# Kernel optimization log

Hardware: AMD Instinct MI355X
Metric: run time of the kernel (lower is better)

## Reference

```python
import jax, jax.numpy as jnp
import numpy as np

KSIZE = (3, 3, 3)
STRIDE = (2, 2, 2)
PAD = (1, 1, 1)
DIL = (1, 1, 1)


def _box_sum(x):
    # Sum over a (kT,kH,kW) window with stride/padding/dilation, applied over
    # the last 3 dims of a [N, C, T, H, W] tensor (equivalent to conv3d with a
    # ones kernel applied channel-wise).
    return jax.lax.reduce_window(
        x,
        jnp.array(0.0, x.dtype),
        jax.lax.add,
        window_dimensions=(1, 1) + KSIZE,
        window_strides=(1, 1) + STRIDE,
        padding=((0, 0), (0, 0)) + tuple((p, p) for p in PAD),
        window_dilation=(1, 1) + DIL,
    )


def setup_inputs() -> dict:
    key = jax.random.key(0)
    k1, k2 = jax.random.split(key)
    vw = jax.random.normal(k1, (4, 256, 16, 56, 56), dtype=jnp.float32)
    w = jax.random.normal(k2, (4, 16, 256), dtype=jnp.float32)
    return {"vw": vw, "w": w}


def reference(vw, w):
    # vw: [N, C, T, H, W] visual words; w: [N, K, C] language words
    C = vw.shape[1]
    # per-word dot products (the 1x1x1 conv3d in the original): [N, K, T, H, W]
    dotp = jnp.einsum('nkc,ncthw->nkthw', w, vw)
    # aggregate over words (op='max'), keepdim -> [N, 1, T, H, W]
    agg = jnp.max(dotp, axis=1, keepdims=True)
    emap = jnp.exp(agg / np.float32(np.sqrt(C)))
    # box-filter sum of exp map -> denominator [N, 1, T', H', W']
    denom = _box_sum(emap)
    # box-filter sum of exp-weighted features -> numerator [N, C, T', H', W']
    num = _box_sum(vw * emap)
    return num / denom
```

## Files before the change

### kernel.cpp

```cpp
#include <hip/hip_runtime.h>
#include <hip/hip_bf16.h>

#define N_  4
#define C_  256
#define K_  16
#define T_  16
#define H_  56
#define W_  56
#define HW_ (H_ * W_)
#define THW_ (T_ * HW_)
#define TP_ 8
#define HP_ 28
#define WP_ 28
#define PP_ (HP_ * WP_)
#define CCHUNK 8

__global__ __launch_bounds__(256) void emap_kernel(const float* __restrict__ vw,
                                                   const float* __restrict__ w,
                                                   float* __restrict__ emap) {
    __shared__ float wl[K_ * C_];
    const int tid = threadIdx.x;
    const int bpn = THW_ / (256 * 2);
    const int n = blockIdx.x / bpn;
    const int lb = blockIdx.x % bpn;

    const float* wn = w + n * (K_ * C_);
#pragma unroll
    for (int i = 0; i < K_; ++i) wl[i * C_ + tid] = wn[i * C_ + tid];
    __syncthreads();

    const int s = (lb * 256 + tid) * 2;
    const float* vbase = vw + (long)n * C_ * THW_ + s;

    float acc0[K_], acc1[K_];
#pragma unroll
    for (int k = 0; k < K_; ++k) { acc0[k] = 0.f; acc1[k] = 0.f; }

    for (int c4 = 0; c4 < C_; c4 += 4) {
        float2 v0 = *(const float2*)(vbase + (long)(c4 + 0) * THW_);
        float2 v1 = *(const float2*)(vbase + (long)(c4 + 1) * THW_);
        float2 v2 = *(const float2*)(vbase + (long)(c4 + 2) * THW_);
        float2 v3 = *(const float2*)(vbase + (long)(c4 + 3) * THW_);
#pragma unroll
        for (int k = 0; k < K_; ++k) {
            float4 wk = *(const float4*)&wl[k * C_ + c4];
            acc0[k] += wk.x * v0.x + wk.y * v1.x + wk.z * v2.x + wk.w * v3.x;
            acc1[k] += wk.x * v0.y + wk.y * v1.y + wk.z * v2.y + wk.w * v3.y;
        }
    }

    float m0 = acc0[0], m1 = acc1[0];
#pragma unroll
    for (int k = 1; k < K_; ++k) { m0 = fmaxf(m0, acc0[k]); m1 = fmaxf(m1, acc1[k]); }

    float2 e;
    e.x = expf(m0 * 0.0625f);
    e.y = expf(m1 * 0.0625f);
    *(float2*)(emap + (long)n * THW_ + s) = e;
}

__global__ __launch_bounds__(256) void box_kernel(const float* __restrict__ vw,
                                                  const float* __restrict__ emap,
                                                  float* __restrict__ out) {
    __shared__ float se[3 * HW_];
    __shared__ float sden[PP_];

    const int tid = threadIdx.x;
    const int cb = blockIdx.x * CCHUNK;
    const int tp = blockIdx.y;
    const int n  = blockIdx.z;
    const int t0 = 2 * tp - 1;

    for (int sl = 0; sl < 3; ++sl) {
        const int tt = t0 + sl;
        if (tt >= 0) {
            const float* src = emap + (long)n * THW_ + (long)tt * HW_;
            for (int i = tid; i < HW_; i += 256) se[sl * HW_ + i] = src[i];
        } else {
            for (int i = tid; i < HW_; i += 256) se[sl * HW_ + i] = 0.f;
        }
    }
    __syncthreads();

    for (int p = tid; p < PP_; p += 256) {
        const int hp = p / WP_, wp = p % WP_;
        const int h0 = 2 * hp - 1, w0 = 2 * wp - 1;
        float ssum = 0.f;
#pragma unroll
        for (int dt = 0; dt < 3; ++dt) {
#pragma unroll
            for (int dh = 0; dh < 3; ++dh) {
                const int h = h0 + dh;
                if (h < 0) continue;
#pragma unroll
                for (int dw = 0; dw < 3; ++dw) {
                    const int w = w0 + dw;
                    if (w < 0) continue;
                    ssum += se[dt * HW_ + h * W_ + w];
                }
            }
        }
        sden[p] = 1.0f / ssum;
    }
    __syncthreads();

    for (int idx = tid; idx < CCHUNK * PP_; idx += 256) {
        const int c = cb + idx / PP_;
        const int p = idx % PP_;
        const int hp = p / WP_, wp = p % WP_;
        const int h0 = 2 * hp - 1, w0 = 2 * wp - 1;
        const float* vbase = vw + ((long)n * C_ + c) * THW_;
        float num = 0.f;
#pragma unroll
        for (int dt = 0; dt < 3; ++dt) {
            const int tt = t0 + dt;
            if (tt < 0) continue;
            const float* vt = vbase + (long)tt * HW_;
            const float* et = se + dt * HW_;
#pragma unroll
            for (int dh = 0; dh < 3; ++dh) {
                const int h = h0 + dh;
                if (h < 0) continue;
#pragma unroll
                for (int dw = 0; dw < 3; ++dw) {
                    const int w = w0 + dw;
                    if (w < 0) continue;
                    const int o = h * W_ + w;
                    num += vt[o] * et[o];
                }
            }
        }
        out[(((long)n * C_ + c) * TP_ + tp) * PP_ + p] = num * sden[p];
    }
}

extern "C" void kernel_launch(void* const* d_in, const int* in_sizes, int n_in,
                              void* d_out, int out_size, void* d_ws, size_t ws_size,
                              hipStream_t stream) {
    const float* vw = (const float*)d_in[0];
    const float* w  = (const float*)d_in[1];
    float* out  = (float*)d_out;
    float* emap = (float*)d_ws;

    emap_kernel<<<392, 256, 0, stream>>>(vw, w, emap);

    box_kernel<<<dim3(C_ / CCHUNK, TP_, N_), 256, 0, stream>>>(vw, emap, out);
}
```

Baseline: 416.8 us.

## Split emap channel reduction across waves and restructure box kernel per output position

The emap kernel now splits the 256-channel dot product across four waves, each covering 64 channels. Partial sums are reduced through shared memory and launched over four times as many blocks, which raises parallelism and occupancy; weights are read directly from global memory instead of being staged in LDS. The box kernel drops the shared-memory staging of three emap slices. Each thread now owns one output position, keeps its 27 emap values and offsets in registers, and loops over 16 channels, so the denominator is computed once per thread and reused. The trade-off is higher register pressure and uncached global gathers of vw with stride-2 access.

```diff
diff --git a/kernel.cpp b/kernel.cpp
--- a/kernel.cpp
+++ b/kernel.cpp
@@ -13,124 +13,115 @@
 #define HP_ 28
 #define WP_ 28
 #define PP_ (HP_ * WP_)
-#define CCHUNK 8
+#define CB_ 16
 
 __global__ __launch_bounds__(256) void emap_kernel(const float* __restrict__ vw,
                                                    const float* __restrict__ w,
                                                    float* __restrict__ emap) {
-    __shared__ float wl[K_ * C_];
-    const int tid = threadIdx.x;
-    const int bpn = THW_ / (256 * 2);
-    const int n = blockIdx.x / bpn;
-    const int lb = blockIdx.x % bpn;
+    __shared__ float part[K_][4][128];
+    const int tid  = threadIdx.x;
+    const int wave = tid >> 6;
+    const int lane = tid & 63;
+    const int bpn  = THW_ / 128;
+    const int n    = blockIdx.x / bpn;
+    const int s0   = (blockIdx.x % bpn) * 128;
+    const int s    = s0 + lane * 2;
 
-    const float* wn = w + n * (K_ * C_);
+    const float* vbase = vw + (long)(n * C_ + wave * 64) * THW_ + s;
+    const float* wn    = w + n * (K_ * C_) + wave * 64;
+
+    float a0[K_], a1[K_];
 #pragma unroll
-    for (int i = 0; i < K_; ++i) wl[i * C_ + tid] = wn[i * C_ + tid];
-    __syncthreads();
+    for (int k = 0; k < K_; ++k) { a0[k] = 0.f; a1[k] = 0.f; }
 
-    const int s = (lb * 256 + tid) * 2;
-    const float* vbase = vw + (long)n * C_ * THW_ + s;
-
-    float acc0[K_], acc1[K_];
-#pragma unroll
-    for (int k = 0; k < K_; ++k) { acc0[k] = 0.f; acc1[k] = 0.f; }
-
-    for (int c4 = 0; c4 < C_; c4 += 4) {
-        float2 v0 = *(const float2*)(vbase + (long)(c4 + 0) * THW_);
-        float2 v1 = *(const float2*)(vbase + (long)(c4 + 1) * THW_);
-        float2 v2 = *(const float2*)(vbase + (long)(c4 + 2) * THW_);
-        float2 v3 = *(const float2*)(vbase + (long)(c4 + 3) * THW_);
+    for (int c = 0; c < 64; c += 4) {
+        float2 v0 = *(const float2*)(vbase + (long)(c + 0) * THW_);
+        float2 v1 = *(const float2*)(vbase + (long)(c + 1) * THW_);
+        float2 v2 = *(const float2*)(vbase + (long)(c + 2) * THW_);
+        float2 v3 = *(const float2*)(vbase + (long)(c + 3) * THW_);
 #pragma unroll
         for (int k = 0; k < K_; ++k) {
-            float4 wk = *(const float4*)&wl[k * C_ + c4];
-            acc0[k] += wk.x * v0.x + wk.y * v1.x + wk.z * v2.x + wk.w * v3.x;
-            acc1[k] += wk.x * v0.y + wk.y * v1.y + wk.z * v2.y + wk.w * v3.y;
+            const float4 wk = *(const float4*)&wn[k * C_ + c];
+            a0[k] += wk.x * v0.x + wk.y * v1.x + wk.z * v2.x + wk.w * v3.x;
+            a1[k] += wk.x * v0.y + wk.y * v1.y + wk.z * v2.y + wk.w * v3.y;
         }
     }
 
-    float m0 = acc0[0], m1 = acc1[0];
 #pragma unroll
-    for (int k = 1; k < K_; ++k) { m0 = fmaxf(m0, acc0[k]); m1 = fmaxf(m1, acc1[k]); }
+    for (int k = 0; k < K_; ++k) {
+        *(float2*)&part[k][wave][lane * 2] = make_float2(a0[k], a1[k]);
+    }
+    __syncthreads();
 
-    float2 e;
-    e.x = expf(m0 * 0.0625f);
-    e.y = expf(m1 * 0.0625f);
-    *(float2*)(emap + (long)n * THW_ + s) = e;
+    const int pos = tid >> 1, kh = tid & 1;
+    float m = -1e30f;
+#pragma unroll
+    for (int j = 0; j < 8; ++j) {
+        const int k = kh * 8 + j;
+        const float sum = part[k][0][pos] + part[k][1][pos]
+                        + part[k][2][pos] + part[k][3][pos];
+        m = fmaxf(m, sum);
+    }
+    m = fmaxf(m, __shfl_xor(m, 1));
+    if (kh == 0) emap[(long)n * THW_ + s0 + pos] = expf(m * 0.0625f);
 }
 
 __global__ __launch_bounds__(256) void box_kernel(const float* __restrict__ vw,
                                                   const float* __restrict__ emap,
                                                   float* __restrict__ out) {
-    __shared__ float se[3 * HW_];
-    __shared__ float sden[PP_];
+    const int gid = blockIdx.x * 256 + threadIdx.x;
+    const int n   = gid / (TP_ * PP_);
+    const int r   = gid % (TP_ * PP_);
+    const int tp  = r / PP_;
+    const int p   = r % PP_;
+    const int hp  = p / WP_, wp = p % WP_;
+    const int t0  = 2 * tp - 1, h0 = 2 * hp - 1, w0 = 2 * wp - 1;
+    const int c0  = blockIdx.y * CB_;
 
-    const int tid = threadIdx.x;
-    const int cb = blockIdx.x * CCHUNK;
-    const int tp = blockIdx.y;
-    const int n  = blockIdx.z;
-    const int t0 = 2 * tp - 1;
+    const float* ebase = emap + (long)n * THW_;
 
-    for (int sl = 0; sl < 3; ++sl) {
-        const int tt = t0 + sl;
-        if (tt >= 0) {
-            const float* src = emap + (long)n * THW_ + (long)tt * HW_;
-            for (int i = tid; i < HW_; i += 256) se[sl * HW_ + i] = src[i];
-        } else {
-            for (int i = tid; i < HW_; i += 256) se[sl * HW_ + i] = 0.f;
+    float e[27];
+    int   off[27];
+    float den = 0.f;
+#pragma unroll
+    for (int dt = 0; dt < 3; ++dt) {
+        const int tt = t0 + dt;
+        const bool tvld = (tt >= 0);
+        const int tc = tvld ? tt : 0;
+#pragma unroll
+        for (int dh = 0; dh < 3; ++dh) {
+            const int h = h0 + dh;
+            const bool hvld = (h >= 0);
+            const int hc = hvld ? h : 0;
+#pragma unroll
+            for (int dw = 0; dw < 3; ++dw) {
+                const int w = w0 + dw;
+                const bool wvld = (w >= 0);
+                const int wc = wvld ? w : 0;
+                const int i = (dt * 3 + dh) * 3 + dw;
+                off[i] = tc * HW_ + hc * W_ + wc;
+                float ev = ebase[off[i]];
+                ev = (tvld && hvld && wvld) ? ev : 0.f;
+                e[i] = ev;
+                den += ev;
+            }
         }
     }
-    __syncthreads();
+    const float rden = 1.0f / den;
 
-    for (int p = tid; p < PP_; p += 256) {
-        const int hp = p / WP_, wp = p % WP_;
-        const int h0 = 2 * hp - 1, w0 = 2 * wp - 1;
-        float ssum = 0.f;
+    const float* vb = vw + ((long)n * C_ + c0) * THW_;
+    float* ob = out + (((long)n * C_ + c0) * TP_ + tp) * PP_ + p;
+
+    for (int c = 0; c < CB_; ++c) {
+        const float* vc = vb + (long)c * THW_;
+        float n0 = 0.f, n1 = 0.f, n2 = 0.f;
 #pragma unroll
-        for (int dt = 0; dt < 3; ++dt) {
-#pragma unroll
-            for (int dh = 0; dh < 3; ++dh) {
-                const int h = h0 + dh;
-                if (h < 0) continue;
-#pragma unroll
-                for (int dw = 0; dw < 3; ++dw) {
-                    const int w = w0 + dw;
-                    if (w < 0) continue;
-                    ssum += se[dt * HW_ + h * W_ + w];
-                }
-            }
+        for (int i = 0; i < 27; i += 3) {
+            n0 += vc[off[i + 0]] * e[i + 0];
+            n1 += vc[off[i + 1]] * e[i + 1];
+            n2 += vc[off[i + 2]] * e[i + 2];
         }
-        sden[p] = 1.0f / ssum;
-    }
-    __syncthreads();
-
-    for (int idx = tid; idx < CCHUNK * PP_; idx += 256) {
-        const int c = cb + idx / PP_;
-        const int p = idx % PP_;
-        const int hp = p / WP_, wp = p % WP_;
-        const int h0 = 2 * hp - 1, w0 = 2 * wp - 1;
-        const float* vbase = vw + ((long)n * C_ + c) * THW_;
-        float num = 0.f;
-#pragma unroll
-        for (int dt = 0; dt < 3; ++dt) {
-            const int tt = t0 + dt;
-            if (tt < 0) continue;
-            const float* vt = vbase + (long)tt * HW_;
-            const float* et = se + dt * HW_;
-#pragma unroll
-            for (int dh = 0; dh < 3; ++dh) {
-                const int h = h0 + dh;
-                if (h < 0) continue;
-#pragma unroll
-                for (int dw = 0; dw < 3; ++dw) {
-                    const int w = w0 + dw;
-                    if (w < 0) continue;
-                    const int o = h * W_ + w;
-                    num += vt[o] * et[o];
-                }
-            }
-        }
-        out[(((long)n * C_ + c) * TP_ + tp) * PP_ + p] = num * sden[p];
+        ob[(long)c * (TP_ * PP_)] = (n0 + n1 + n2) * rden;
     }
 }
 
@@ -142,7 +133,7 @@
     float* out  = (float*)d_out;
     float* emap = (float*)d_ws;
 
-    emap_kernel<<<392, 256, 0, stream>>>(vw, w, emap);
+    emap_kernel<<<1568, 256, 0, stream>>>(vw, w, emap);
 
-    box_kernel<<<dim3(C_ / CCHUNK, TP_, N_), 256, 0, stream>>>(vw, emap, out);
+    box_kernel<<<dim3(98, C_ / CB_), 256, 0, stream>>>(vw, emap, out);
 }
```

Result: slower. 535.0 us (+28.3%).

## Split channel reduction across waves, precompute denominators, stage weighted slices in LDS

Applied to the files above, without the earlier changes.

The emap kernel now gives each wave a quarter of the channels with float4 loads over four spatial points, then reduces the per-wave partial dot products through shared memory before the max and exp. A separate small kernel computes the reciprocal box-sum denominators once per output position instead of once per block. The box kernel now handles one channel per block. It loads vw*emap slices into LDS with coalesced float4 reads, so the 27-tap window reads come from LDS rather than scattered global loads. This trades an extra launch and more blocks for better coalescing and less redundant denominator work.

```diff
diff --git a/kernel.cpp b/kernel.cpp
--- a/kernel.cpp
+++ b/kernel.cpp
@@ -13,124 +13,169 @@
 #define HP_ 28
 #define WP_ 28
 #define PP_ (HP_ * WP_)
-#define CCHUNK 8
 
 __global__ __launch_bounds__(256) void emap_kernel(const float* __restrict__ vw,
                                                    const float* __restrict__ w,
                                                    float* __restrict__ emap) {
-    __shared__ float wl[K_ * C_];
-    const int tid = threadIdx.x;
-    const int bpn = THW_ / (256 * 2);
-    const int n = blockIdx.x / bpn;
-    const int lb = blockIdx.x % bpn;
+    __shared__ float wt[C_ * K_];
+    __shared__ float part[8][4][256];
+
+    const int tid  = threadIdx.x;
+    const int wv   = tid >> 6;
+    const int lane = tid & 63;
+    const int bpn  = THW_ / 256;
+    const int n    = blockIdx.x / bpn;
+    const int s0   = (blockIdx.x % bpn) * 256;
 
     const float* wn = w + n * (K_ * C_);
 #pragma unroll
-    for (int i = 0; i < K_; ++i) wl[i * C_ + tid] = wn[i * C_ + tid];
+    for (int k = 0; k < K_; ++k) wt[tid * K_ + k] = wn[k * C_ + tid];
     __syncthreads();
 
-    const int s = (lb * 256 + tid) * 2;
-    const float* vbase = vw + (long)n * C_ * THW_ + s;
+    const float* vbase = vw + (long)(n * C_ + wv * 64) * THW_ + s0 + (lane << 2);
 
-    float acc0[K_], acc1[K_];
+    float a[K_][4];
 #pragma unroll
-    for (int k = 0; k < K_; ++k) { acc0[k] = 0.f; acc1[k] = 0.f; }
+    for (int k = 0; k < K_; ++k)
+#pragma unroll
+        for (int p = 0; p < 4; ++p) a[k][p] = 0.f;
 
-    for (int c4 = 0; c4 < C_; c4 += 4) {
-        float2 v0 = *(const float2*)(vbase + (long)(c4 + 0) * THW_);
-        float2 v1 = *(const float2*)(vbase + (long)(c4 + 1) * THW_);
-        float2 v2 = *(const float2*)(vbase + (long)(c4 + 2) * THW_);
-        float2 v3 = *(const float2*)(vbase + (long)(c4 + 3) * THW_);
+#pragma unroll 2
+    for (int g = 0; g < 16; ++g) {
+        float4 vv[4];
 #pragma unroll
-        for (int k = 0; k < K_; ++k) {
-            float4 wk = *(const float4*)&wl[k * C_ + c4];
-            acc0[k] += wk.x * v0.x + wk.y * v1.x + wk.z * v2.x + wk.w * v3.x;
-            acc1[k] += wk.x * v0.y + wk.y * v1.y + wk.z * v2.y + wk.w * v3.y;
+        for (int j = 0; j < 4; ++j)
+            vv[j] = *(const float4*)(vbase + (long)(g * 4 + j) * THW_);
+#pragma unroll
+        for (int j = 0; j < 4; ++j) {
+            const int c = wv * 64 + g * 4 + j;
+#pragma unroll
+            for (int kk = 0; kk < 4; ++kk) {
+                const float4 wk = *(const float4*)&wt[c * K_ + kk * 4];
+#define FMA4(Q, WC) \
+                a[kk*4+Q][0] += (WC) * vv[j].x; a[kk*4+Q][1] += (WC) * vv[j].y; \
+                a[kk*4+Q][2] += (WC) * vv[j].z; a[kk*4+Q][3] += (WC) * vv[j].w;
+                FMA4(0, wk.x) FMA4(1, wk.y) FMA4(2, wk.z) FMA4(3, wk.w)
+#undef FMA4
+            }
         }
     }
 
-    float m0 = acc0[0], m1 = acc1[0];
+    float m = -3.4e38f;
 #pragma unroll
-    for (int k = 1; k < K_; ++k) { m0 = fmaxf(m0, acc0[k]); m1 = fmaxf(m1, acc1[k]); }
+    for (int kc = 0; kc < 2; ++kc) {
+#pragma unroll
+        for (int kq = 0; kq < 8; ++kq) {
+            *(float4*)&part[kq][wv][lane * 4] =
+                make_float4(a[kc*8+kq][0], a[kc*8+kq][1], a[kc*8+kq][2], a[kc*8+kq][3]);
+        }
+        __syncthreads();
+        float ml = -3.4e38f;
+#pragma unroll
+        for (int kq = 0; kq < 8; ++kq) {
+            const float s = part[kq][0][tid] + part[kq][1][tid]
+                          + part[kq][2][tid] + part[kq][3][tid];
+            ml = fmaxf(ml, s);
+        }
+        m = fmaxf(m, ml);
+        __syncthreads();
+    }
 
-    float2 e;
-    e.x = expf(m0 * 0.0625f);
-    e.y = expf(m1 * 0.0625f);
-    *(float2*)(emap + (long)n * THW_ + s) = e;
+    emap[(long)n * THW_ + s0 + tid] = expf(m * 0.0625f);
+}
+
+__global__ __launch_bounds__(256) void rden_kernel(const float* __restrict__ emap,
+                                                   float* __restrict__ rden) {
+    const int gid = blockIdx.x * 256 + threadIdx.x;
+    const int n   = gid / (TP_ * PP_);
+    const int r   = gid % (TP_ * PP_);
+    const int tp  = r / PP_;
+    const int p   = r % PP_;
+    const int hp  = p / WP_, wp = p % WP_;
+    const int t0  = 2 * tp - 1, h0 = 2 * hp - 1, w0 = 2 * wp - 1;
+    const float* eb = emap + (long)n * THW_;
+
+    float den = 0.f;
+#pragma unroll
+    for (int dt = 0; dt < 3; ++dt) {
+        const int tt = t0 + dt;
+        const bool tv = (tt >= 0);
+        const int tc = tv ? tt : 0;
+#pragma unroll
+        for (int dh = 0; dh < 3; ++dh) {
+            const int h = h0 + dh;
+            const bool hv = tv && (h >= 0);
+            const int hc = (h >= 0) ? h : 0;
+#pragma unroll
+            for (int dw = 0; dw < 3; ++dw) {
+                const int w = w0 + dw;
+                const bool v = hv && (w >= 0);
+                const int wc = (w >= 0) ? w : 0;
+                const float ev = eb[tc * HW_ + hc * W_ + wc];
+                den += v ? ev : 0.f;
+            }
+        }
+    }
+    rden[gid] = 1.0f / den;
 }
 
 __global__ __launch_bounds__(256) void box_kernel(const float* __restrict__ vw,
                                                   const float* __restrict__ emap,
+                                                  const float* __restrict__ rden,
                                                   float* __restrict__ out) {
-    __shared__ float se[3 * HW_];
-    __shared__ float sden[PP_];
+    __shared__ float sp[3][HW_];
+    __shared__ float sr[PP_];
 
     const int tid = threadIdx.x;
-    const int cb = blockIdx.x * CCHUNK;
-    const int tp = blockIdx.y;
-    const int n  = blockIdx.z;
-    const int t0 = 2 * tp - 1;
+    const int c   = blockIdx.x;
+    const int tp  = blockIdx.y;
+    const int n   = blockIdx.z;
+    const int t0  = 2 * tp - 1;
 
+    const float* eb = emap + (long)n * THW_;
+    const float* vb = vw + (long)(n * C_ + c) * THW_;
+
+#pragma unroll
     for (int sl = 0; sl < 3; ++sl) {
         const int tt = t0 + sl;
         if (tt >= 0) {
-            const float* src = emap + (long)n * THW_ + (long)tt * HW_;
-            for (int i = tid; i < HW_; i += 256) se[sl * HW_ + i] = src[i];
+            const float4* vs = (const float4*)(vb + tt * HW_);
+            const float4* es = (const float4*)(eb + tt * HW_);
+            for (int i = tid; i < HW_ / 4; i += 256) {
+                const float4 v = vs[i], e = es[i];
+                *(float4*)&sp[sl][i * 4] =
+                    make_float4(v.x * e.x, v.y * e.y, v.z * e.z, v.w * e.w);
+            }
         } else {
-            for (int i = tid; i < HW_; i += 256) se[sl * HW_ + i] = 0.f;
+            for (int i = tid; i < HW_ / 4; i += 256)
+                *(float4*)&sp[sl][i * 4] = make_float4(0.f, 0.f, 0.f, 0.f);
         }
     }
+    const float* rt = rden + (n * TP_ + tp) * PP_;
+    for (int i = tid; i < PP_; i += 256) sr[i] = rt[i];
     __syncthreads();
 
+    float* ob = out + (((long)(n * C_ + c)) * TP_ + tp) * PP_;
     for (int p = tid; p < PP_; p += 256) {
         const int hp = p / WP_, wp = p % WP_;
         const int h0 = 2 * hp - 1, w0 = 2 * wp - 1;
-        float ssum = 0.f;
+        float num = 0.f;
 #pragma unroll
-        for (int dt = 0; dt < 3; ++dt) {
+        for (int dh = 0; dh < 3; ++dh) {
+            const int h = h0 + dh;
+            const bool hv = (h >= 0);
+            const int hc = hv ? h : 0;
 #pragma unroll
-            for (int dh = 0; dh < 3; ++dh) {
-                const int h = h0 + dh;
-                if (h < 0) continue;
-#pragma unroll
-                for (int dw = 0; dw < 3; ++dw) {
-                    const int w = w0 + dw;
-                    if (w < 0) continue;
-                    ssum += se[dt * HW_ + h * W_ + w];
-                }
+            for (int dw = 0; dw < 3; ++dw) {
+                const int w = w0 + dw;
+                const bool v = hv && (w >= 0);
+                const int wc = (w >= 0) ? w : 0;
+                const int o = hc * W_ + wc;
+                const float s3 = sp[0][o] + sp[1][o] + sp[2][o];
+                num += v ? s3 : 0.f;
             }
         }
-        sden[p] = 1.0f / ssum;
-    }
-    __syncthreads();
-
-    for (int idx = tid; idx < CCHUNK * PP_; idx += 256) {
-        const int c = cb + idx / PP_;
-        const int p = idx % PP_;
-        const int hp = p / WP_, wp = p % WP_;
-        const int h0 = 2 * hp - 1, w0 = 2 * wp - 1;
-        const float* vbase = vw + ((long)n * C_ + c) * THW_;
-        float num = 0.f;
-#pragma unroll
-        for (int dt = 0; dt < 3; ++dt) {
-            const int tt = t0 + dt;
-            if (tt < 0) continue;
-            const float* vt = vbase + (long)tt * HW_;
-            const float* et = se + dt * HW_;
-#pragma unroll
-            for (int dh = 0; dh < 3; ++dh) {
-                const int h = h0 + dh;
-                if (h < 0) continue;
-#pragma unroll
-                for (int dw = 0; dw < 3; ++dw) {
-                    const int w = w0 + dw;
-                    if (w < 0) continue;
-                    const int o = h * W_ + w;
-                    num += vt[o] * et[o];
-                }
-            }
-        }
-        out[(((long)n * C_ + c) * TP_ + tp) * PP_ + p] = num * sden[p];
+        ob[p] = num * sr[p];
     }
 }
 
@@ -141,8 +186,11 @@
     const float* w  = (const float*)d_in[1];
     float* out  = (float*)d_out;
     float* emap = (float*)d_ws;
+    float* rden = emap + (long)N_ * THW_;
 
-    emap_kernel<<<392, 256, 0, stream>>>(vw, w, emap);
+    emap_kernel<<<784, 256, 0, stream>>>(vw, w, emap);
 
-    box_kernel<<<dim3(C_ / CCHUNK, TP_, N_), 256, 0, stream>>>(vw, emap, out);
+    rden_kernel<<<98, 256, 0, stream>>>(emap, rden);
+
+    box_kernel<<<dim3(C_, TP_, N_), 256, 0, stream>>>(vw, emap, rden, out);
 }
```

New measurement: 343.9 us. 17.5% less time.
